# Performance work log

Hardware: AMD Instinct MI355X
Metric: run time of the kernel (lower is better)

## Reference

```python
import jax, jax.numpy as jnp
import numpy as np

B, SEQ, DIM = 4, 2048, 2048
NH, HD = 16, 128            # head_dim = dim // n_head
HID = 5632                  # int(2*(4*dim)/3) rounded up to multiple_of=256
EPS = 1e-5
THETA = 500000.0


def setup_inputs() -> dict:
    key = jax.random.key(0)
    ks = jax.random.split(key, 9)
    s = 0.02  # init scale keeps activations/logits well-conditioned
    x = jax.random.normal(ks[0], (B, SEQ, DIM), jnp.float32)
    wq = jax.random.normal(ks[1], (DIM, DIM), jnp.float32) * s
    wk = jax.random.normal(ks[2], (DIM, DIM), jnp.float32) * s
    wv = jax.random.normal(ks[3], (DIM, DIM), jnp.float32) * s
    wo = jax.random.normal(ks[4], (DIM, DIM), jnp.float32) * s
    w1 = jax.random.normal(ks[5], (DIM, HID), jnp.float32) * s
    w2 = jax.random.normal(ks[6], (HID, DIM), jnp.float32) * s
    w3 = jax.random.normal(ks[7], (DIM, HID), jnp.float32) * s
    attn_norm_w = jnp.ones((DIM,), jnp.float32)
    ffn_norm_w = jnp.ones((DIM,), jnp.float32)
    # RoPE tables (real/imag of freqs_cis), [seq, head_dim//2]
    inv = 1.0 / (THETA ** (jnp.arange(0, HD, 2, dtype=jnp.float32) / HD))
    ang = jnp.arange(SEQ, dtype=jnp.float32)[:, None] * inv[None, :]
    return dict(x=x, wq=wq, wk=wk, wv=wv, wo=wo, w1=w1, w2=w2, w3=w3,
                attn_norm_w=attn_norm_w, ffn_norm_w=ffn_norm_w,
                freqs_cos=jnp.cos(ang), freqs_sin=jnp.sin(ang))


def rmsnorm(x, w, eps=EPS):
    return x * jax.lax.rsqrt(jnp.mean(x * x, axis=-1, keepdims=True) + eps) * w


def rope(x, cos, sin):
    # x: [b, s, h, d]; pairs (d0,d1),(d2,d3),... treated as complex, multiplied by e^{i*ang}
    a, b = x[..., 0::2], x[..., 1::2]
    c = cos[None, :, None, :]
    s = sin[None, :, None, :]
    return jnp.stack([a * c - b * s, a * s + b * c], axis=-1).reshape(x.shape)


def block(x, wq, wk, wv, wo, w1, w2, w3, attn_norm_w, ffn_norm_w, freqs_cos, freqs_sin):
    b, s, d = x.shape
    # --- attention sublayer ---
    hn = rmsnorm(x, attn_norm_w)
    q = (hn @ wq).reshape(b, s, NH, HD)
    k = (hn @ wk).reshape(b, s, NH, HD)
    v = (hn @ wv).reshape(b, s, NH, HD)
    q = rope(q, freqs_cos, freqs_sin)
    k = rope(k, freqs_cos, freqs_sin)
    scores = jnp.einsum('bqhd,bkhd->bhqk', q, k) / np.float32(np.sqrt(HD))
    mask = jnp.triu(jnp.full((s, s), -jnp.inf, dtype=scores.dtype), k=1)
    p = jax.nn.softmax(scores + mask, axis=-1)
    attn = jnp.einsum('bhqk,bkhd->bqhd', p, v).reshape(b, s, d) @ wo
    h = x + attn
    # --- SwiGLU FFN sublayer ---
    fn = rmsnorm(h, ffn_norm_w)
    ffn = (jax.nn.silu(fn @ w1) * (fn @ w3)) @ w2
    return h + ffn


def reference(x, wq, wk, wv, wo, w1, w2, w3, attn_norm_w, ffn_norm_w, freqs_cos, freqs_sin):
    return block(x, wq, wk, wv, wo, w1, w2, w3, attn_norm_w, ffn_norm_w, freqs_cos, freqs_sin)
```

## Files before the change

kernel.cpp:

```cpp
#include <hip/hip_runtime.h>
#include <stdint.h>

#define DIMV 2048
#define SEQV 2048
#define NHV 16
#define HDV 128
#define HIDV 5632
#define NROWS 8192
#define LDP 6144

typedef short bf16x8 __attribute__((ext_vector_type(8)));
typedef float f32x4 __attribute__((ext_vector_type(4)));
typedef unsigned short u16x8 __attribute__((ext_vector_type(8)));

#define GLD16(src, dst) __builtin_amdgcn_global_load_lds( \
    (const __attribute__((address_space(1))) unsigned int*)(src), \
    (__attribute__((address_space(3))) unsigned int*)(dst), 16, 0, 0)

__device__ __forceinline__ float bf2f(unsigned short u){
  union { unsigned u; float f; } x; x.u = ((unsigned)u) << 16; return x.f;
}
__device__ __forceinline__ unsigned short f2bf(float f){
  union { float f; unsigned u; } x; x.f = f;
  unsigned r = x.u + 0x7fffu + ((x.u >> 16) & 1u);
  return (unsigned short)(r >> 16);
}

__global__ void transpose_cast(const float* __restrict__ in, unsigned short* __restrict__ out,
                               int R, int C){
  __shared__ alignas(16) unsigned short tile[32][33];
  int c0 = blockIdx.x * 32, r0 = blockIdx.y * 32;
  int tx = threadIdx.x, ty = threadIdx.y;
#pragma unroll
  for (int i = 0; i < 32; i += 8)
    tile[ty + i][tx] = f2bf(in[(long)(r0 + ty + i) * C + (c0 + tx)]);
  __syncthreads();
#pragma unroll
  for (int i = 0; i < 32; i += 8)
    out[(long)(c0 + ty + i) * R + (r0 + tx)] = tile[tx][ty + i];
}

__global__ void transpose_v(const unsigned short* __restrict__ packed, unsigned short* __restrict__ vt){
  __shared__ alignas(16) unsigned short tile[32][33];
  int bh = blockIdx.z;
  int b = bh >> 4, h = bh & 15;
  int d0 = blockIdx.y * 32, s0 = blockIdx.x * 32;
  int tx = threadIdx.x, ty = threadIdx.y;
  const unsigned short* src = packed + (long)b * SEQV * LDP + 4096 + (long)h * HDV;
  unsigned short* dst = vt + (long)bh * HDV * SEQV;
#pragma unroll
  for (int i = 0; i < 32; i += 8)
    tile[ty + i][tx] = src[(long)(s0 + ty + i) * LDP + d0 + tx];
  __syncthreads();
#pragma unroll
  for (int i = 0; i < 32; i += 8)
    dst[(long)(d0 + ty + i) * SEQV + s0 + tx] = tile[tx][ty + i];
}

__global__ __launch_bounds__(256) void rmsnorm_k(const float* __restrict__ x,
                                                 const float* __restrict__ w,
                                                 unsigned short* __restrict__ out){
  int row = blockIdx.x, t = threadIdx.x;
  const float* xr = x + (long)row * DIMV;
  float4 v0 = ((const float4*)xr)[t * 2];
  float4 v1 = ((const float4*)xr)[t * 2 + 1];
  float ss = v0.x*v0.x + v0.y*v0.y + v0.z*v0.z + v0.w*v0.w
           + v1.x*v1.x + v1.y*v1.y + v1.z*v1.z + v1.w*v1.w;
#pragma unroll
  for (int off = 32; off; off >>= 1) ss += __shfl_down(ss, off);
  __shared__ float red[4];
  if ((t & 63) == 0) red[t >> 6] = ss;
  __syncthreads();
  float tot = red[0] + red[1] + red[2] + red[3];
  float sc = rsqrtf(tot * (1.0f / DIMV) + 1e-5f);
  const float* wr = w + t * 8;
  float vv[8] = {v0.x, v0.y, v0.z, v0.w, v1.x, v1.y, v1.z, v1.w};
  u16x8 o;
#pragma unroll
  for (int e = 0; e < 8; e++) o[e] = f2bf(vv[e] * sc * wr[e]);
  *(u16x8*)(out + (long)row * DIMV + t * 8) = o;
}

template <int MODE>
__global__ __launch_bounds__(512, 2) void gemm256(const unsigned short* __restrict__ A, int lda,
                                                  const unsigned short* __restrict__ Bt,
                                                  unsigned short* __restrict__ Cb,
                                                  float* __restrict__ Cf,
                                                  const float* __restrict__ resid,
                                                  int ldc, int M, int N, int K){
  __shared__ alignas(16) unsigned short As[2][256 * 64];
  __shared__ alignas(16) unsigned short Bs[2][256 * 64];
  int m0 = blockIdx.y * 256, n0 = blockIdx.x * 256;
  int tid = threadIdx.x, w = tid >> 6, l = tid & 63;
  int wm = w >> 2, wn = w & 3;
  int l15 = l & 15, l4 = l >> 4;
  int srow = tid >> 3;
  int scol = (tid & 7) * 8;

  f32x4 acc[8][4];
#pragma unroll
  for (int i = 0; i < 8; i++)
#pragma unroll
    for (int j = 0; j < 4; j++) acc[i][j] = (f32x4){0.f, 0.f, 0.f, 0.f};

  int nt = K / 64;
#define G256_STAGE(buf, kt) {                                                     \
    int k0 = (kt) * 64;                                                           \
    _Pragma("unroll")                                                             \
    for (int j = 0; j < 4; j++){                                                  \
      GLD16(A + (long)(m0 + j * 64 + srow) * lda + k0 + scol,                     \
            As[buf] + j * 4096 + w * 512);                                        \
      GLD16(Bt + (long)(n0 + j * 64 + srow) * K + k0 + scol,                      \
            Bs[buf] + j * 4096 + w * 512);                                        \
    } }

  G256_STAGE(0, 0);
  asm volatile("s_waitcnt vmcnt(0)" ::: "memory");
  __syncthreads();
  int cur = 0;
  for (int t = 0; t < nt; t++){
    if (t + 1 < nt) G256_STAGE(cur ^ 1, t + 1);
#pragma unroll
    for (int ksub = 0; ksub < 2; ksub++){
      bf16x8 bfr[4];
#pragma unroll
      for (int ni = 0; ni < 4; ni++)
        bfr[ni] = *(const bf16x8*)(Bs[cur] + (wn * 64 + ni * 16 + l15) * 64 + ksub * 32 + l4 * 8);
#pragma unroll
      for (int mi = 0; mi < 8; mi++){
        bf16x8 af = *(const bf16x8*)(As[cur] + (wm * 128 + mi * 16 + l15) * 64 + ksub * 32 + l4 * 8);
#pragma unroll
        for (int ni = 0; ni < 4; ni++)
          acc[mi][ni] = __builtin_amdgcn_mfma_f32_16x16x32_bf16(af, bfr[ni], acc[mi][ni], 0, 0, 0);
      }
    }
    asm volatile("s_waitcnt vmcnt(0)" ::: "memory");
    __syncthreads();
    cur ^= 1;
  }
#pragma unroll
  for (int mi = 0; mi < 8; mi++)
#pragma unroll
    for (int ni = 0; ni < 4; ni++)
#pragma unroll
      for (int r = 0; r < 4; r++){
        int row = m0 + wm * 128 + mi * 16 + l4 * 4 + r;
        int col = n0 + wn * 64 + ni * 16 + l15;
        long idx = (long)row * ldc + col;
        float v = acc[mi][ni][r];
        if (MODE == 0) Cb[idx] = f2bf(v);
        else           Cf[idx] = v + resid[idx];
      }
#undef G256_STAGE
}

__global__ __launch_bounds__(512, 2) void ffn13_256(const unsigned short* __restrict__ A,
                                                    const unsigned short* __restrict__ B1t,
                                                    const unsigned short* __restrict__ B3t,
                                                    unsigned short* __restrict__ G,
                                                    int M, int N, int K){
  __shared__ alignas(16) unsigned short As[2][256 * 64];
  __shared__ alignas(16) unsigned short B1s[2][128 * 64];
  __shared__ alignas(16) unsigned short B3s[2][128 * 64];
  int m0 = blockIdx.y * 256, n0 = blockIdx.x * 128;
  int tid = threadIdx.x, w = tid >> 6, l = tid & 63;
  int wm = w >> 2, wn = w & 3;
  int l15 = l & 15, l4 = l >> 4;
  int srow = tid >> 3;
  int scol = (tid & 7) * 8;

  f32x4 acc1[8][2], acc3[8][2];
#pragma unroll
  for (int i = 0; i < 8; i++)
#pragma unroll
    for (int j = 0; j < 2; j++){ acc1[i][j] = (f32x4){0.f,0.f,0.f,0.f}; acc3[i][j] = (f32x4){0.f,0.f,0.f,0.f}; }

  int nt = K / 64;
#define F13_STAGE(buf, kt) {                                                      \
    int k0 = (kt) * 64;                                                           \
    _Pragma("unroll")                                                             \
    for (int j = 0; j < 4; j++)                                                   \
      GLD16(A + (long)(m0 + j * 64 + srow) * K + k0 + scol,                       \
            As[buf] + j * 4096 + w * 512);                                        \
    _Pragma("unroll")                                                             \
    for (int j = 0; j < 2; j++){                                                  \
      GLD16(B1t + (long)(n0 + j * 64 + srow) * K + k0 + scol,                     \
            B1s[buf] + j * 4096 + w * 512);                                       \
      GLD16(B3t + (long)(n0 + j * 64 + srow) * K + k0 + scol,                     \
            B3s[buf] + j * 4096 + w * 512);                                       \
    } }

  F13_STAGE(0, 0);
  asm volatile("s_waitcnt vmcnt(0)" ::: "memory");
  __syncthreads();
  int cur = 0;
  for (int t = 0; t < nt; t++){
    if (t + 1 < nt) F13_STAGE(cur ^ 1, t + 1);
#pragma unroll
    for (int ksub = 0; ksub < 2; ksub++){
      bf16x8 b1f[2], b3f[2];
#pragma unroll
      for (int ni = 0; ni < 2; ni++){
        b1f[ni] = *(const bf16x8*)(B1s[cur] + (wn * 32 + ni * 16 + l15) * 64 + ksub * 32 + l4 * 8);
        b3f[ni] = *(const bf16x8*)(B3s[cur] + (wn * 32 + ni * 16 + l15) * 64 + ksub * 32 + l4 * 8);
      }
#pragma unroll
      for (int mi = 0; mi < 8; mi++){
        bf16x8 af = *(const bf16x8*)(As[cur] + (wm * 128 + mi * 16 + l15) * 64 + ksub * 32 + l4 * 8);
#pragma unroll
        for (int ni = 0; ni < 2; ni++){
          acc1[mi][ni] = __builtin_amdgcn_mfma_f32_16x16x32_bf16(af, b1f[ni], acc1[mi][ni], 0, 0, 0);
          acc3[mi][ni] = __builtin_amdgcn_mfma_f32_16x16x32_bf16(af, b3f[ni], acc3[mi][ni], 0, 0, 0);
        }
      }
    }
    asm volatile("s_waitcnt vmcnt(0)" ::: "memory");
    __syncthreads();
    cur ^= 1;
  }
#pragma unroll
  for (int mi = 0; mi < 8; mi++)
#pragma unroll
    for (int ni = 0; ni < 2; ni++)
#pragma unroll
      for (int r = 0; r < 4; r++){
        int row = m0 + wm * 128 + mi * 16 + l4 * 4 + r;
        int col = n0 + wn * 32 + ni * 16 + l15;
        float a = acc1[mi][ni][r];
        float si = a * (1.f / (1.f + __expf(-a)));
        G[(long)row * N + col] = f2bf(si * acc3[mi][ni][r]);
      }
#undef F13_STAGE
}

__global__ __launch_bounds__(256) void rope_k(unsigned short* __restrict__ p,
                                              const float* __restrict__ cosT,
                                              const float* __restrict__ sinT,
                                              float qscale){
  long idx = (long)blockIdx.x * 256 + threadIdx.x;
  int i = (int)(idx & 63);
  long t = idx >> 6;
  int h = (int)(t & 15);
  long row = t >> 4;
  int s = (int)(row & (SEQV - 1));
  float c = cosT[s * 64 + i], sn = sinT[s * 64 + i];
  long base = row * LDP + h * HDV + 2 * i;
  unsigned pq = *(unsigned*)(p + base);
  float a = bf2f((unsigned short)(pq & 0xffff)), b = bf2f((unsigned short)(pq >> 16));
  float ra = (a * c - b * sn) * qscale, rb = (a * sn + b * c) * qscale;
  *(unsigned*)(p + base) = (unsigned)f2bf(ra) | ((unsigned)f2bf(rb) << 16);
  unsigned pk = *(unsigned*)(p + base + 2048);
  a = bf2f((unsigned short)(pk & 0xffff)); b = bf2f((unsigned short)(pk >> 16));
  ra = a * c - b * sn; rb = a * sn + b * c;
  *(unsigned*)(p + base + 2048) = (unsigned)f2bf(ra) | ((unsigned)f2bf(rb) << 16);
}

__global__ __launch_bounds__(256) void attn_k(unsigned short* __restrict__ p,
                                              const unsigned short* __restrict__ vt){
  __shared__ alignas(16) unsigned short Ks[2][64 * 128];
  __shared__ alignas(16) unsigned short Vs[2][128 * 64];
  __shared__ alignas(16) unsigned short Ps[4][16 * 64];
  int qt = (gridDim.x - 1) - blockIdx.x;
  int bh = blockIdx.y;
  int b = bh >> 4, h = bh & 15;
  int tid = threadIdx.x, w = tid >> 6, l = tid & 63;
  int l15 = l & 15, l4 = l >> 4;
  int qrow0 = qt * 64 + w * 16;
  long baseQ = (long)b * SEQV * LDP + (long)h * HDV;
  long baseV = (long)bh * HDV * SEQV;

  bf16x8 qf[4];
#pragma unroll
  for (int dc = 0; dc < 4; dc++)
    qf[dc] = *(const bf16x8*)(p + baseQ + (long)(qrow0 + l15) * LDP + dc * 32 + l4 * 8);

  f32x4 acc[8];
#pragma unroll
  for (int df = 0; df < 8; df++) acc[df] = (f32x4){0.f, 0.f, 0.f, 0.f};
  float mOld[4], lsum[4];
#pragma unroll
  for (int r = 0; r < 4; r++){ mOld[r] = -1e30f; lsum[r] = 0.f; }

#define ATTN_STAGE(buf, kt) {                                                       \
    int k0 = (kt) * 64;                                                             \
    _Pragma("unroll")                                                               \
    for (int i = 0; i < 4; i++){                                                    \
      int row = w * 16 + i * 4 + (l >> 4);                                          \
      int slot = (l & 15) ^ (row & 7);                                              \
      GLD16(p + baseQ + 2048 + (long)(k0 + row) * LDP + slot * 8,                   \
            Ks[buf] + (w * 16 + i * 4) * 128);                                      \
    }                                                                               \
    _Pragma("unroll")                                                               \
    for (int i = 0; i < 4; i++){                                                    \
      int row = w * 32 + i * 8 + (l >> 3);                                          \
      int slot = (l & 7) ^ (row & 7);                                               \
      GLD16(vt + baseV + (long)row * SEQV + k0 + slot * 8,                          \
            Vs[buf] + (w * 32 + i * 8) * 64);                                       \
    } }

  int ntile = qt + 1;
  ATTN_STAGE(0, 0);
  asm volatile("s_waitcnt vmcnt(0)" ::: "memory");
  __syncthreads();
  int cur = 0;
  for (int tki = 0; tki < ntile; tki++){
    int k0 = tki * 64;
    if (tki + 1 < ntile) ATTN_STAGE(cur ^ 1, tki + 1);

    float s[4][4];
    __builtin_amdgcn_s_setprio(1);
#pragma unroll
    for (int kf = 0; kf < 4; kf++){
      f32x4 sf = (f32x4){0.f, 0.f, 0.f, 0.f};
#pragma unroll
      for (int dc = 0; dc < 4; dc++){
        bf16x8 kb = *(const bf16x8*)(Ks[cur] + (kf * 16 + l15) * 128 + (((dc * 4 + l4) ^ (l15 & 7)) * 8));
        sf = __builtin_amdgcn_mfma_f32_16x16x32_bf16(qf[dc], kb, sf, 0, 0, 0);
      }
      int key = k0 + kf * 16 + l15;
#pragma unroll
      for (int r = 0; r < 4; r++){
        int rowi = qrow0 + l4 * 4 + r;
        s[kf][r] = (key <= rowi) ? sf[r] : -1e30f;
      }
    }
    __builtin_amdgcn_s_setprio(0);
    float scale[4];
#pragma unroll
    for (int r = 0; r < 4; r++){
      float vmax = fmaxf(fmaxf(s[0][r], s[1][r]), fmaxf(s[2][r], s[3][r]));
      for (int mm = 8; mm; mm >>= 1) vmax = fmaxf(vmax, __shfl_xor(vmax, mm));
      float mNew = fmaxf(mOld[r], vmax);
      scale[r] = __expf(mOld[r] - mNew);
      float ps = 0.f;
#pragma unroll
      for (int kf = 0; kf < 4; kf++){
        float pp = __expf(s[kf][r] - mNew);
        s[kf][r] = pp;
        ps += pp;
      }
      for (int mm = 8; mm; mm >>= 1) ps += __shfl_xor(ps, mm);
      lsum[r] = lsum[r] * scale[r] + ps;
      mOld[r] = mNew;
    }
#pragma unroll
    for (int df = 0; df < 8; df++)
#pragma unroll
      for (int r = 0; r < 4; r++) acc[df][r] *= scale[r];
#pragma unroll
    for (int kf = 0; kf < 4; kf++)
#pragma unroll
      for (int r = 0; r < 4; r++){
        int row = l4 * 4 + r;
        int sidx = row * 64 + (((((kf * 16 + l15) * 2)) ^ ((row & 7) << 4)) >> 1);
        Ps[w][sidx] = f2bf(s[kf][r]);
      }
    __builtin_amdgcn_s_setprio(1);
#pragma unroll
    for (int kc = 0; kc < 2; kc++){
      bf16x8 pa = *(const bf16x8*)(Ps[w] + l15 * 64 + (((kc * 64 + l4 * 16) ^ ((l15 & 7) << 4)) >> 1));
#pragma unroll
      for (int df = 0; df < 8; df++){
        bf16x8 vb = *(const bf16x8*)(Vs[cur] + (df * 16 + l15) * 64 + (((kc * 4 + l4) ^ (l15 & 7)) * 8));
        acc[df] = __builtin_amdgcn_mfma_f32_16x16x32_bf16(pa, vb, acc[df], 0, 0, 0);
      }
    }
    __builtin_amdgcn_s_setprio(0);
    asm volatile("s_waitcnt vmcnt(0)" ::: "memory");
    __syncthreads();
    cur ^= 1;
  }
#pragma unroll
  for (int df = 0; df < 8; df++)
#pragma unroll
    for (int r = 0; r < 4; r++){
      int rows = qrow0 + l4 * 4 + r;
      p[baseQ + (long)rows * LDP + df * 16 + l15] = f2bf(acc[df][r] / lsum[r]);
    }
#undef ATTN_STAGE
}

extern "C" void kernel_launch(void* const* d_in, const int* in_sizes, int n_in,
                              void* d_out, int out_size, void* d_ws, size_t ws_size,
                              hipStream_t stream){
  const float* x    = (const float*)d_in[0];
  const float* wq   = (const float*)d_in[1];
  const float* wk   = (const float*)d_in[2];
  const float* wv   = (const float*)d_in[3];
  const float* wo   = (const float*)d_in[4];
  const float* w1   = (const float*)d_in[5];
  const float* w2   = (const float*)d_in[6];
  const float* w3   = (const float*)d_in[7];
  const float* anw  = (const float*)d_in[8];
  const float* fnw  = (const float*)d_in[9];
  const float* fcos = (const float*)d_in[10];
  const float* fsin = (const float*)d_in[11];

  char* ws = (char*)d_ws;
  size_t off = 0;
  auto alloc = [&](size_t bytes) -> void* {
    void* p = ws + off;
    off += (bytes + 255) & ~(size_t)255;
    return p;
  };
  const size_t SQ = (size_t)DIMV * DIMV * 2;
  const size_t SW = (size_t)DIMV * HIDV * 2;
  const size_t SA = (size_t)NROWS * DIMV * 2;
  const size_t SP = (size_t)NROWS * LDP * 2;

  unsigned short* wqT = (unsigned short*)alloc(SQ);
  unsigned short* wkT = (unsigned short*)alloc(SQ);
  unsigned short* wvT = (unsigned short*)alloc(SQ);
  unsigned short* woT = (unsigned short*)alloc(SQ);
  unsigned short* w1T = (unsigned short*)alloc(SW);
  unsigned short* w3T = (unsigned short*)alloc(SW);
  unsigned short* w2T = (unsigned short*)alloc(SW);
  unsigned short* hn  = (unsigned short*)alloc(SA);
  unsigned short* pk  = (unsigned short*)alloc(SP);
  unsigned short* vtb = hn;
  unsigned short* g   = pk;
  float* hf = (float*)d_out;
  (void)ws_size; (void)in_sizes; (void)n_in; (void)out_size;
  (void)wkT; (void)wvT;

  dim3 tb(32, 8);
  transpose_cast<<<dim3(DIMV/32, DIMV/32), tb, 0, stream>>>(wq, wqT, DIMV, DIMV);
  transpose_cast<<<dim3(DIMV/32, DIMV/32), tb, 0, stream>>>(wk, wkT, DIMV, DIMV);
  transpose_cast<<<dim3(DIMV/32, DIMV/32), tb, 0, stream>>>(wv, wvT, DIMV, DIMV);
  transpose_cast<<<dim3(DIMV/32, DIMV/32), tb, 0, stream>>>(wo, woT, DIMV, DIMV);
  transpose_cast<<<dim3(HIDV/32, DIMV/32), tb, 0, stream>>>(w1, w1T, DIMV, HIDV);
  transpose_cast<<<dim3(HIDV/32, DIMV/32), tb, 0, stream>>>(w3, w3T, DIMV, HIDV);
  transpose_cast<<<dim3(DIMV/32, HIDV/32), tb, 0, stream>>>(w2, w2T, HIDV, DIMV);

  rmsnorm_k<<<NROWS, 256, 0, stream>>>(x, anw, hn);

  gemm256<0><<<dim3(LDP/256, NROWS/256), 512, 0, stream>>>(hn, DIMV, wqT, pk, nullptr, nullptr, LDP, NROWS, LDP, DIMV);

  rope_k<<<(NROWS * NHV * 64) / 256, 256, 0, stream>>>(pk, fcos, fsin, 0.08838834764831845f);

  transpose_v<<<dim3(SEQV/32, HDV/32, 4 * NHV), tb, 0, stream>>>(pk, vtb);

  attn_k<<<dim3(SEQV/64, 4 * NHV), 256, 0, stream>>>(pk, vtb);

  gemm256<1><<<dim3(DIMV/256, NROWS/256), 512, 0, stream>>>(pk, LDP, woT, nullptr, hf, x, DIMV, NROWS, DIMV, DIMV);

  rmsnorm_k<<<NROWS, 256, 0, stream>>>(hf, fnw, hn);

  ffn13_256<<<dim3(HIDV/128, NROWS/256), 512, 0, stream>>>(hn, w1T, w3T, g, NROWS, HIDV, DIMV);

  gemm256<1><<<dim3(DIMV/256, NROWS/256), 512, 0, stream>>>(g, HIDV, w2T, nullptr, hf, (const float*)hf, DIMV, NROWS, DIMV, HIDV);
}
```

Measured before the change: 1.542 ms.

## Restructure GEMM main loops into 8-wave ping-pong schedule with swizzled LDS

Both the generic 256x256 GEMM and the fused FFN w1/w3 kernel are rewritten so each K-tile is split into four MFMA clusters. Global-to-LDS loads for half-tiles are interleaved between the clusters, separated by raw s_barriers, s_setprio and partial vmcnt waits. A-halves are issued one to two tiles ahead. LDS rows are also XOR-swizzled at 16-byte granularity to avoid bank conflicts on fragment reads. The goal is to hide global load latency and LDS conflicts behind MFMA work, at the cost of more barriers and intricate buffer-reuse ordering that could race if the vmcnt accounting is off.

```diff
diff --git a/kernel.cpp b/kernel.cpp
--- a/kernel.cpp
+++ b/kernel.cpp
@@ -94,8 +94,8 @@
   int tid = threadIdx.x, w = tid >> 6, l = tid & 63;
   int wm = w >> 2, wn = w & 3;
   int l15 = l & 15, l4 = l >> 4;
-  int srow = tid >> 3;
-  int scol = (tid & 7) * 8;
+  int sr8 = l >> 3, sl = l & 7;
+  int nt = K / 64;
 
   f32x4 acc[8][4];
 #pragma unroll
@@ -103,41 +103,93 @@
 #pragma unroll
     for (int j = 0; j < 4; j++) acc[i][j] = (f32x4){0.f, 0.f, 0.f, 0.f};
 
-  int nt = K / 64;
-#define G256_STAGE(buf, kt) {                                                     \
-    int k0 = (kt) * 64;                                                           \
-    _Pragma("unroll")                                                             \
-    for (int j = 0; j < 4; j++){                                                  \
-      GLD16(A + (long)(m0 + j * 64 + srow) * lda + k0 + scol,                     \
-            As[buf] + j * 4096 + w * 512);                                        \
-      GLD16(Bt + (long)(n0 + j * 64 + srow) * K + k0 + scol,                      \
-            Bs[buf] + j * 4096 + w * 512);                                        \
+#define GSTAGE(Gp, ld_, r0_, slab) { \
+    _Pragma("unroll") \
+    for (int r = 0; r < 2; r++){ \
+      int row = (r * 8 + w) * 8 + sr8; \
+      int cs = sl ^ (row & 7); \
+      GLD16((Gp) + (long)((r0_) + row) * (ld_) + cs * 8, (slab) + (r * 8 + w) * 512); \
     } }
-
-  G256_STAGE(0, 0);
-  asm volatile("s_waitcnt vmcnt(0)" ::: "memory");
+#define STAGE_A(tt, half) { int _t = (tt); if (_t < nt) GSTAGE(A + _t * 64, lda, m0 + (half) * 128, &As[_t & 1][(half) * 8192]) }
+#define STAGE_B(tt, half) { int _t = (tt); if (_t < nt) GSTAGE(Bt + _t * 64, K, n0 + (half) * 128, &Bs[_t & 1][(half) * 8192]) }
+#define LDA8(mi, ks) (*(const bf16x8*)(&As[bi][(wm * 128 + (mi) * 16 + l15) * 64 + (((ks) * 4 + l4) ^ (l15 & 7)) * 8]))
+#define LDB8(ni, ks) (*(const bf16x8*)(&Bs[bi][(wn * 64 + (ni) * 16 + l15) * 64 + (((ks) * 4 + l4) ^ (l15 & 7)) * 8]))
+
+  STAGE_A(0, 0); STAGE_A(0, 1); STAGE_B(0, 0); STAGE_B(0, 1);
+  STAGE_A(1, 0); STAGE_B(1, 0); STAGE_B(1, 1);
+  asm volatile("s_waitcnt vmcnt(6)" ::: "memory");
   __syncthreads();
-  int cur = 0;
+
   for (int t = 0; t < nt; t++){
-    if (t + 1 < nt) G256_STAGE(cur ^ 1, t + 1);
-#pragma unroll
-    for (int ksub = 0; ksub < 2; ksub++){
-      bf16x8 bfr[4];
-#pragma unroll
-      for (int ni = 0; ni < 4; ni++)
-        bfr[ni] = *(const bf16x8*)(Bs[cur] + (wn * 64 + ni * 16 + l15) * 64 + ksub * 32 + l4 * 8);
-#pragma unroll
-      for (int mi = 0; mi < 8; mi++){
-        bf16x8 af = *(const bf16x8*)(As[cur] + (wm * 128 + mi * 16 + l15) * 64 + ksub * 32 + l4 * 8);
-#pragma unroll
-        for (int ni = 0; ni < 4; ni++)
-          acc[mi][ni] = __builtin_amdgcn_mfma_f32_16x16x32_bf16(af, bfr[ni], acc[mi][ni], 0, 0, 0);
-      }
-    }
-    asm volatile("s_waitcnt vmcnt(0)" ::: "memory");
-    __syncthreads();
-    cur ^= 1;
+    int bi = t & 1;
+    bf16x8 af[8][2], bf0[2][2], bf1[2][2];
+#pragma unroll
+    for (int mi = 0; mi < 8; mi++){ af[mi][0] = LDA8(mi, 0); af[mi][1] = LDA8(mi, 1); }
+#pragma unroll
+    for (int ni = 0; ni < 2; ni++){ bf0[ni][0] = LDB8(ni, 0); bf0[ni][1] = LDB8(ni, 1); }
+    STAGE_A(t + 1, 1);
+    __builtin_amdgcn_s_barrier();
+    asm volatile("s_waitcnt lgkmcnt(0)" ::: "memory");
+    __builtin_amdgcn_sched_barrier(0);
+    __builtin_amdgcn_s_setprio(1);
+#pragma unroll
+    for (int mi = 0; mi < 4; mi++)
+#pragma unroll
+      for (int ni = 0; ni < 2; ni++)
+#pragma unroll
+        for (int ks = 0; ks < 2; ks++)
+          acc[mi][ni] = __builtin_amdgcn_mfma_f32_16x16x32_bf16(af[mi][ks], bf0[ni][ks], acc[mi][ni], 0, 0, 0);
+    __builtin_amdgcn_s_setprio(0);
+    __builtin_amdgcn_s_barrier();
+#pragma unroll
+    for (int ni = 0; ni < 2; ni++){ bf1[ni][0] = LDB8(ni + 2, 0); bf1[ni][1] = LDB8(ni + 2, 1); }
+    STAGE_A(t + 2, 0);
+    __builtin_amdgcn_s_barrier();
+    asm volatile("s_waitcnt lgkmcnt(0)" ::: "memory");
+    __builtin_amdgcn_sched_barrier(0);
+    __builtin_amdgcn_s_setprio(1);
+#pragma unroll
+    for (int mi = 4; mi < 8; mi++)
+#pragma unroll
+      for (int ni = 0; ni < 2; ni++)
+#pragma unroll
+        for (int ks = 0; ks < 2; ks++)
+          acc[mi][ni] = __builtin_amdgcn_mfma_f32_16x16x32_bf16(af[mi][ks], bf0[ni][ks], acc[mi][ni], 0, 0, 0);
+    __builtin_amdgcn_s_setprio(0);
+    __builtin_amdgcn_s_barrier();
+    STAGE_B(t + 2, 0);
+    __builtin_amdgcn_s_barrier();
+    __builtin_amdgcn_s_setprio(1);
+#pragma unroll
+    for (int mi = 0; mi < 4; mi++)
+#pragma unroll
+      for (int ni = 0; ni < 2; ni++)
+#pragma unroll
+        for (int ks = 0; ks < 2; ks++)
+          acc[mi][ni + 2] = __builtin_amdgcn_mfma_f32_16x16x32_bf16(af[mi][ks], bf1[ni][ks], acc[mi][ni + 2], 0, 0, 0);
+    __builtin_amdgcn_s_setprio(0);
+    __builtin_amdgcn_s_barrier();
+    STAGE_B(t + 2, 1);
+    __builtin_amdgcn_s_barrier();
+    __builtin_amdgcn_s_setprio(1);
+#pragma unroll
+    for (int mi = 4; mi < 8; mi++)
+#pragma unroll
+      for (int ni = 0; ni < 2; ni++)
+#pragma unroll
+        for (int ks = 0; ks < 2; ks++)
+          acc[mi][ni + 2] = __builtin_amdgcn_mfma_f32_16x16x32_bf16(af[mi][ks], bf1[ni][ks], acc[mi][ni + 2], 0, 0, 0);
+    __builtin_amdgcn_s_setprio(0);
+    if (t + 2 < nt) asm volatile("s_waitcnt vmcnt(6)" ::: "memory");
+    else            asm volatile("s_waitcnt vmcnt(0)" ::: "memory");
+    __builtin_amdgcn_s_barrier();
   }
+#undef GSTAGE
+#undef STAGE_A
+#undef STAGE_B
+#undef LDA8
+#undef LDB8
+
 #pragma unroll
   for (int mi = 0; mi < 8; mi++)
 #pragma unroll
@@ -151,7 +203,6 @@
         if (MODE == 0) Cb[idx] = f2bf(v);
         else           Cf[idx] = v + resid[idx];
       }
-#undef G256_STAGE
 }
 
 __global__ __launch_bounds__(512, 2) void ffn13_256(const unsigned short* __restrict__ A,
@@ -166,8 +217,8 @@
   int tid = threadIdx.x, w = tid >> 6, l = tid & 63;
   int wm = w >> 2, wn = w & 3;
   int l15 = l & 15, l4 = l >> 4;
-  int srow = tid >> 3;
-  int scol = (tid & 7) * 8;
+  int sr8 = l >> 3, sl = l & 7;
+  int nt = K / 64;
 
   f32x4 acc1[8][2], acc3[8][2];
 #pragma unroll
@@ -175,49 +226,97 @@
 #pragma unroll
     for (int j = 0; j < 2; j++){ acc1[i][j] = (f32x4){0.f,0.f,0.f,0.f}; acc3[i][j] = (f32x4){0.f,0.f,0.f,0.f}; }
 
-  int nt = K / 64;
-#define F13_STAGE(buf, kt) {                                                      \
-    int k0 = (kt) * 64;                                                           \
-    _Pragma("unroll")                                                             \
-    for (int j = 0; j < 4; j++)                                                   \
-      GLD16(A + (long)(m0 + j * 64 + srow) * K + k0 + scol,                       \
-            As[buf] + j * 4096 + w * 512);                                        \
-    _Pragma("unroll")                                                             \
-    for (int j = 0; j < 2; j++){                                                  \
-      GLD16(B1t + (long)(n0 + j * 64 + srow) * K + k0 + scol,                     \
-            B1s[buf] + j * 4096 + w * 512);                                       \
-      GLD16(B3t + (long)(n0 + j * 64 + srow) * K + k0 + scol,                     \
-            B3s[buf] + j * 4096 + w * 512);                                       \
+#define GSTAGE(Gp, ld_, r0_, slab) { \
+    _Pragma("unroll") \
+    for (int r = 0; r < 2; r++){ \
+      int row = (r * 8 + w) * 8 + sr8; \
+      int cs = sl ^ (row & 7); \
+      GLD16((Gp) + (long)((r0_) + row) * (ld_) + cs * 8, (slab) + (r * 8 + w) * 512); \
     } }
-
-  F13_STAGE(0, 0);
-  asm volatile("s_waitcnt vmcnt(0)" ::: "memory");
+#define STAGE_A(tt, half) { int _t = (tt); if (_t < nt) GSTAGE(A + _t * 64, K, m0 + (half) * 128, &As[_t & 1][(half) * 8192]) }
+#define STAGE_B1(tt) { int _t = (tt); if (_t < nt) GSTAGE(B1t + _t * 64, K, n0, &B1s[_t & 1][0]) }
+#define STAGE_B3(tt) { int _t = (tt); if (_t < nt) GSTAGE(B3t + _t * 64, K, n0, &B3s[_t & 1][0]) }
+#define LDA8(mi, ks) (*(const bf16x8*)(&As[bi][(wm * 128 + (mi) * 16 + l15) * 64 + (((ks) * 4 + l4) ^ (l15 & 7)) * 8]))
+#define LDB18(ni, ks) (*(const bf16x8*)(&B1s[bi][(wn * 32 + (ni) * 16 + l15) * 64 + (((ks) * 4 + l4) ^ (l15 & 7)) * 8]))
+#define LDB38(ni, ks) (*(const bf16x8*)(&B3s[bi][(wn * 32 + (ni) * 16 + l15) * 64 + (((ks) * 4 + l4) ^ (l15 & 7)) * 8]))
+
+  STAGE_A(0, 0); STAGE_A(0, 1); STAGE_B1(0); STAGE_B3(0);
+  STAGE_A(1, 0); STAGE_B1(1); STAGE_B3(1);
+  asm volatile("s_waitcnt vmcnt(6)" ::: "memory");
   __syncthreads();
-  int cur = 0;
+
   for (int t = 0; t < nt; t++){
-    if (t + 1 < nt) F13_STAGE(cur ^ 1, t + 1);
-#pragma unroll
-    for (int ksub = 0; ksub < 2; ksub++){
-      bf16x8 b1f[2], b3f[2];
-#pragma unroll
-      for (int ni = 0; ni < 2; ni++){
-        b1f[ni] = *(const bf16x8*)(B1s[cur] + (wn * 32 + ni * 16 + l15) * 64 + ksub * 32 + l4 * 8);
-        b3f[ni] = *(const bf16x8*)(B3s[cur] + (wn * 32 + ni * 16 + l15) * 64 + ksub * 32 + l4 * 8);
-      }
-#pragma unroll
-      for (int mi = 0; mi < 8; mi++){
-        bf16x8 af = *(const bf16x8*)(As[cur] + (wm * 128 + mi * 16 + l15) * 64 + ksub * 32 + l4 * 8);
-#pragma unroll
-        for (int ni = 0; ni < 2; ni++){
-          acc1[mi][ni] = __builtin_amdgcn_mfma_f32_16x16x32_bf16(af, b1f[ni], acc1[mi][ni], 0, 0, 0);
-          acc3[mi][ni] = __builtin_amdgcn_mfma_f32_16x16x32_bf16(af, b3f[ni], acc3[mi][ni], 0, 0, 0);
-        }
-      }
-    }
-    asm volatile("s_waitcnt vmcnt(0)" ::: "memory");
-    __syncthreads();
-    cur ^= 1;
+    int bi = t & 1;
+    bf16x8 af[8][2], b1f[2][2], b3f[2][2];
+#pragma unroll
+    for (int mi = 0; mi < 8; mi++){ af[mi][0] = LDA8(mi, 0); af[mi][1] = LDA8(mi, 1); }
+#pragma unroll
+    for (int ni = 0; ni < 2; ni++){ b1f[ni][0] = LDB18(ni, 0); b1f[ni][1] = LDB18(ni, 1); }
+    STAGE_A(t + 1, 1);
+    __builtin_amdgcn_s_barrier();
+    asm volatile("s_waitcnt lgkmcnt(0)" ::: "memory");
+    __builtin_amdgcn_sched_barrier(0);
+    __builtin_amdgcn_s_setprio(1);
+#pragma unroll
+    for (int mi = 0; mi < 4; mi++)
+#pragma unroll
+      for (int ni = 0; ni < 2; ni++)
+#pragma unroll
+        for (int ks = 0; ks < 2; ks++)
+          acc1[mi][ni] = __builtin_amdgcn_mfma_f32_16x16x32_bf16(af[mi][ks], b1f[ni][ks], acc1[mi][ni], 0, 0, 0);
+    __builtin_amdgcn_s_setprio(0);
+    __builtin_amdgcn_s_barrier();
+#pragma unroll
+    for (int ni = 0; ni < 2; ni++){ b3f[ni][0] = LDB38(ni, 0); b3f[ni][1] = LDB38(ni, 1); }
+    STAGE_A(t + 2, 0);
+    __builtin_amdgcn_s_barrier();
+    asm volatile("s_waitcnt lgkmcnt(0)" ::: "memory");
+    __builtin_amdgcn_sched_barrier(0);
+    __builtin_amdgcn_s_setprio(1);
+#pragma unroll
+    for (int mi = 4; mi < 8; mi++)
+#pragma unroll
+      for (int ni = 0; ni < 2; ni++)
+#pragma unroll
+        for (int ks = 0; ks < 2; ks++)
+          acc1[mi][ni] = __builtin_amdgcn_mfma_f32_16x16x32_bf16(af[mi][ks], b1f[ni][ks], acc1[mi][ni], 0, 0, 0);
+    __builtin_amdgcn_s_setprio(0);
+    __builtin_amdgcn_s_barrier();
+    STAGE_B1(t + 2);
+    __builtin_amdgcn_s_barrier();
+    __builtin_amdgcn_s_setprio(1);
+#pragma unroll
+    for (int mi = 0; mi < 4; mi++)
+#pragma unroll
+      for (int ni = 0; ni < 2; ni++)
+#pragma unroll
+        for (int ks = 0; ks < 2; ks++)
+          acc3[mi][ni] = __builtin_amdgcn_mfma_f32_16x16x32_bf16(af[mi][ks], b3f[ni][ks], acc3[mi][ni], 0, 0, 0);
+    __builtin_amdgcn_s_setprio(0);
+    __builtin_amdgcn_s_barrier();
+    STAGE_B3(t + 2);
+    __builtin_amdgcn_s_barrier();
+    __builtin_amdgcn_s_setprio(1);
+#pragma unroll
+    for (int mi = 4; mi < 8; mi++)
+#pragma unroll
+      for (int ni = 0; ni < 2; ni++)
+#pragma unroll
+        for (int ks = 0; ks < 2; ks++)
+          acc3[mi][ni] = __builtin_amdgcn_mfma_f32_16x16x32_bf16(af[mi][ks], b3f[ni][ks], acc3[mi][ni], 0, 0, 0);
+    __builtin_amdgcn_s_setprio(0);
+    if (t + 2 < nt) asm volatile("s_waitcnt vmcnt(6)" ::: "memory");
+    else            asm volatile("s_waitcnt vmcnt(0)" ::: "memory");
+    __builtin_amdgcn_s_barrier();
   }
+#undef GSTAGE
+#undef STAGE_A
+#undef STAGE_B1
+#undef STAGE_B3
+#undef LDA8
+#undef LDB18
+#undef LDB38
+
 #pragma unroll
   for (int mi = 0; mi < 8; mi++)
 #pragma unroll
@@ -230,7 +329,6 @@
         float si = a * (1.f / (1.f + __expf(-a)));
         G[(long)row * N + col] = f2bf(si * acc3[mi][ni][r]);
       }
-#undef F13_STAGE
 }
 
 __global__ __launch_bounds__(256) void rope_k(unsigned short* __restrict__ p,
```

Result: faster. 1.276 ms (-17.2%).
